# Kernel optimization log

Measured on AMD Instinct MI355X. Metric: run time of the kernel, lower is better.

The kernel has to match this reference:

```python
import jax, jax.numpy as jnp
import numpy as np

B, N, C, H, NC = 8, 4096, 512, 256, 1000
GRID = 64  # N = GRID*GRID unique positions
LN_EPS = 1e-5


def setup_inputs() -> dict:
    key = jax.random.key(0)
    ks = jax.random.split(key, 10)
    # unique integer grid positions, same for every batch element (original order)
    i = jnp.arange(N)
    base = jnp.stack([i % GRID, i // GRID], axis=-1).astype(jnp.float32)  # [N,2]
    pos_org = jnp.broadcast_to(base, (B, N, 2))
    # per-batch random permutation -> shuffled positions (as the backbone would emit)
    perm = jax.vmap(lambda k: jax.random.permutation(k, N))(jax.random.split(ks[0], B))  # [B,N]
    pos_shuffled = jnp.take_along_axis(pos_org, perm[..., None], axis=1)
    s = 0.02
    return {
        "feat": jax.random.normal(ks[1], (B, N, C), jnp.float32),
        "prev_out": jax.random.normal(ks[2], (B, N, C), jnp.float32),
        "pos_org": pos_org,
        "pos_shuffled": pos_shuffled,
        "proj_W": jax.random.normal(ks[3], (C, C), jnp.float32) * s,
        "proj_b": jnp.zeros((C,), jnp.float32),
        "ln_g": jnp.ones((C,), jnp.float32),
        "ln_b": jnp.zeros((C,), jnp.float32),
        "W1": jax.random.normal(ks[4], (H, C), jnp.float32) * s,
        "b1": jnp.zeros((H,), jnp.float32),
        "W2": jax.random.normal(ks[5], (H, H), jnp.float32) * s,
        "b2": jnp.zeros((H,), jnp.float32),
        "W3": jax.random.normal(ks[6], (NC, H), jnp.float32) * s,
        "b3": jnp.zeros((NC,), jnp.float32),
    }


def _layernorm(x, g, b):
    x32 = x.astype(jnp.float32)
    mu = x32.mean(-1, keepdims=True)
    var = ((x32 - mu) ** 2).mean(-1, keepdims=True)
    return (x32 - mu) * jax.lax.rsqrt(var + LN_EPS) * g + b


def reference(feat, prev_out, pos_org, pos_shuffled, proj_W, proj_b,
              ln_g, ln_b, W1, b1, W2, b2, W3, b3):
    # find_pos_org_order: L1 cdist [B,N,N] + argmin over shuffled axis
    dists = jnp.abs(pos_org[:, :, None, :] - pos_shuffled[:, None, :, :]).sum(-1)
    pos_indices = jnp.argmin(dists, axis=2)  # [B,N]
    # batched gather: feat[b_, pos_indices]
    g = jnp.take_along_axis(feat, pos_indices[..., None], axis=1)  # [B,N,C]
    # fused proj -> layernorm (in fp32) -> cast back -> residual add
    proj = jnp.einsum('bnc,dc->bnd', g, proj_W) + proj_b
    out_feat = prev_out + _layernorm(proj, ln_g, ln_b).astype(feat.dtype)
    # mean-pool over tokens, 3-layer MLP head with relu on first two layers
    pooled = out_feat.mean(1)  # [B,C]
    h = jax.nn.relu(pooled @ W1.T + b1)
    h = jax.nn.relu(h @ W2.T + b2)
    return h @ W3.T + b3  # [B, num_classes]
```

## Files before the change

kernel.cpp:

```cpp
#include <hip/hip_runtime.h>
#include <stdint.h>

#define B_ 8
#define N_ 4096
#define C_ 512
#define H_ 256
#define NC_ 1000

typedef float v4f __attribute__((ext_vector_type(4)));
typedef short v8s __attribute__((ext_vector_type(8)));
typedef unsigned short ushort_t;

__device__ __forceinline__ uint32_t f2bf1(float f) {
    uint32_t u = __float_as_uint(f);
    return (u + 0x7FFFu + ((u >> 16) & 1u)) >> 16;
}
__device__ __forceinline__ uint32_t pk2(float lo, float hi) {
#if __has_builtin(__builtin_amdgcn_cvt_pk_bf16_f32)
    auto r = __builtin_amdgcn_cvt_pk_bf16_f32(lo, hi);
    return __builtin_bit_cast(uint32_t, r);
#else
    return f2bf1(lo) | (f2bf1(hi) << 16);
#endif
}

__global__ void prep_kernel(const float* __restrict__ ps, const float* __restrict__ W,
                            int* __restrict__ inv, ushort_t* __restrict__ Wfrag,
                            float* __restrict__ pooled) {
    int blk = blockIdx.x, t = threadIdx.x;
    if (blk == 0) {
        float4 z = {0.f, 0.f, 0.f, 0.f};
#pragma unroll
        for (int i = 0; i < 4; i++) ((float4*)pooled)[t * 4 + i] = z;
    }
    if (blk < 128) {
        int gid = blk * 256 + t;
        float2 p = ((const float2*)ps)[gid];
        int key = (int)(p.x + 0.5f) + 64 * (int)(p.y + 0.5f);
        int b = gid >> 12;
        inv[(b << 12) + key] = gid & 4095;
    } else {
        int i = (blk - 128) * 256 + t;
        int d = i >> 6, kb = (i >> 2) & 15, q = i & 3;
        const float4* src = (const float4*)(W + d * C_ + kb * 32 + q * 8);
        float4 v0 = src[0], v1 = src[1];
        uint4 pk;
        pk.x = pk2(v0.x, v0.y); pk.y = pk2(v0.z, v0.w);
        pk.z = pk2(v1.x, v1.y); pk.w = pk2(v1.z, v1.w);
        ((uint4*)Wfrag)[((d >> 4) * 16 + kb) * 64 + q * 16 + (d & 15)] = pk;
    }
}

__global__ __launch_bounds__(512, 4)
void gemm_ln_pool(const float* __restrict__ feat, const float* __restrict__ prev,
                  const int* __restrict__ inv, const ushort_t* __restrict__ Wfrag,
                  const float* __restrict__ pb, const float* __restrict__ lg,
                  const float* __restrict__ lb, float* __restrict__ pooled) {
    __shared__ v8s Abuf[4096];
    __shared__ float RowS[64], RowQ[64], ColS[512];

    const int bid = blockIdx.x;
    const int t = threadIdx.x;

    if (bid % 3 == 2) {
        const int p = bid / 3;
        const int b = p >> 5;
        const int r0 = (p & 31) << 7;
        const float* psrc = prev + ((size_t)(b * N_ + r0) * C_) + t;
        float s0 = 0.f, s1 = 0.f, s2 = 0.f, s3 = 0.f;
#pragma unroll 4
        for (int r = 0; r < 128; r += 4) {
            s0 += psrc[(r + 0) * C_];
            s1 += psrc[(r + 1) * C_];
            s2 += psrc[(r + 2) * C_];
            s3 += psrc[(r + 3) * C_];
        }
        atomicAdd(&pooled[b * C_ + t], (s0 + s1) + (s2 + s3));
        return;
    }

    const int gix = (bid / 3) * 2 + (bid % 3);
    const int b = gix >> 6;
    const int row0 = (gix & 63) << 6;
    const int wv = t >> 6, lane = t & 63, c = lane & 15, q = lane >> 4;

    if (t < 64) { RowS[t] = 0.f; RowQ[t] = 0.f; }

    const int arow = t >> 3;
    const int acol8 = t & 7;
    const int grow = inv[(b << 12) + row0 + arow];
    const float* asrc = feat + ((size_t)(b * N_ + grow) * C_);
#pragma unroll 4
    for (int s = 0; s < 8; s++) {
        const int chunk = s * 8 + acol8;
        float4 f0 = ((const float4*)asrc)[chunk * 2];
        float4 f1 = ((const float4*)asrc)[chunk * 2 + 1];
        uint4 pk;
        pk.x = pk2(f0.x, f0.y); pk.y = pk2(f0.z, f0.w);
        pk.z = pk2(f1.x, f1.y); pk.w = pk2(f1.z, f1.w);
        ((uint4*)Abuf)[arow * 64 + (chunk ^ (arow & 7))] = pk;
    }

    const ushort_t* fb[4];
#pragma unroll
    for (int nt = 0; nt < 4; nt++)
        fb[nt] = Wfrag + (wv * 4 + nt) * 8192 + lane * 8;

    v4f acc[4][4];
    const v4f vzero = {0.f, 0.f, 0.f, 0.f};
#pragma unroll
    for (int mt = 0; mt < 4; mt++)
#pragma unroll
        for (int nt = 0; nt < 4; nt++) acc[mt][nt] = vzero;

    __syncthreads();

#pragma unroll 2
    for (int kb = 0; kb < 16; kb++) {
        v8s af[4], bf[4];
#pragma unroll
        for (int nt = 0; nt < 4; nt++)
            bf[nt] = *((const v8s*)(fb[nt] + kb * 512));
#pragma unroll
        for (int mt = 0; mt < 4; mt++)
            af[mt] = Abuf[(mt * 16 + c) * 64 + ((kb * 4 + q) ^ (c & 7))];
#pragma unroll
        for (int mt = 0; mt < 4; mt++)
#pragma unroll
            for (int nt = 0; nt < 4; nt++)
                acc[mt][nt] = __builtin_amdgcn_mfma_f32_16x16x32_bf16(
                    af[mt], bf[nt], acc[mt][nt], 0, 0, 0);
    }

    float pb4[4], lg4[4], lb4[4];
#pragma unroll
    for (int nt = 0; nt < 4; nt++) {
        int n = wv * 64 + nt * 16 + c;
        pb4[nt] = pb[n]; lg4[nt] = lg[n]; lb4[nt] = lb[n];
    }
#pragma unroll
    for (int mt = 0; mt < 4; mt++) {
#pragma unroll
        for (int reg = 0; reg < 4; reg++) {
            float s1 = 0.f, s2 = 0.f;
#pragma unroll
            for (int nt = 0; nt < 4; nt++) {
                float v = acc[mt][nt][reg] + pb4[nt];
                acc[mt][nt][reg] = v;
                s1 += v; s2 += v * v;
            }
#pragma unroll
            for (int d = 1; d < 16; d <<= 1) {
                s1 += __shfl_xor(s1, d);
                s2 += __shfl_xor(s2, d);
            }
            if (c == 0) {
                int r = mt * 16 + q * 4 + reg;
                atomicAdd(&RowS[r], s1);
                atomicAdd(&RowQ[r], s2);
            }
        }
    }
    __syncthreads();
    if (t < 64) {
        float mu = RowS[t] * (1.f / C_);
        float var = RowQ[t] * (1.f / C_) - mu * mu;
        RowS[t] = mu;
        RowQ[t] = rsqrtf(var + 1e-5f);
    }
    __syncthreads();
    float col[4] = {0.f, 0.f, 0.f, 0.f};
#pragma unroll
    for (int mt = 0; mt < 4; mt++) {
#pragma unroll
        for (int reg = 0; reg < 4; reg++) {
            int r = mt * 16 + q * 4 + reg;
            float mu = RowS[r], rs = RowQ[r];
#pragma unroll
            for (int nt = 0; nt < 4; nt++)
                col[nt] += (acc[mt][nt][reg] - mu) * rs * lg4[nt] + lb4[nt];
        }
    }
#pragma unroll
    for (int nt = 0; nt < 4; nt++) {
        col[nt] += __shfl_xor(col[nt], 16);
        col[nt] += __shfl_xor(col[nt], 32);
    }
    if (lane < 16) {
#pragma unroll
        for (int nt = 0; nt < 4; nt++) ColS[wv * 64 + nt * 16 + c] = col[nt];
    }
    __syncthreads();
    atomicAdd(&pooled[b * C_ + t], ColS[t]);
}

__global__ __launch_bounds__(256)
void head_kernel(const float* __restrict__ pooled,
                 const float* __restrict__ W1, const float* __restrict__ b1,
                 const float* __restrict__ W2, const float* __restrict__ b2,
                 const float* __restrict__ W3, const float* __restrict__ b3,
                 float* __restrict__ out) {
    __shared__ __align__(16) float P[512];
    __shared__ __align__(16) float H1[256];
    __shared__ __align__(16) float H2[256];
    const int t = threadIdx.x, wv = t >> 6, lane = t & 63;
    const int b = blockIdx.x / 25;
    const int slice = blockIdx.x % 25;

    P[t] = pooled[b * C_ + t] * (1.f / 4096.f);
    P[t + 256] = pooled[b * C_ + t + 256] * (1.f / 4096.f);
    __syncthreads();

    {
        const float4* wr = (const float4*)(W1 + t * C_);
        float s = 0.f;
#pragma unroll 8
        for (int k = 0; k < 128; k++) {
            float4 w = wr[k];
            float4 p = ((const float4*)P)[k];
            s += w.x * p.x + w.y * p.y + w.z * p.z + w.w * p.w;
        }
        H1[t] = fmaxf(s + b1[t], 0.f);
    }
    __syncthreads();

    {
        const float4* wr = (const float4*)(W2 + t * H_);
        float s = 0.f;
#pragma unroll 8
        for (int k = 0; k < 64; k++) {
            float4 w = wr[k];
            float4 p = ((const float4*)H1)[k];
            s += w.x * p.x + w.y * p.y + w.z * p.z + w.w * p.w;
        }
        H2[t] = fmaxf(s + b2[t], 0.f);
    }
    __syncthreads();

#pragma unroll
    for (int jj = 0; jj < 10; jj++) {
        const int o = slice * 40 + jj * 4 + wv;
        float4 w = ((const float4*)(W3 + o * H_))[lane];
        float4 p = ((const float4*)H2)[lane];
        float s = w.x * p.x + w.y * p.y + w.z * p.z + w.w * p.w;
#pragma unroll
        for (int d = 1; d < 64; d <<= 1) s += __shfl_xor(s, d);
        if (lane == 0) out[b * NC_ + o] = s + b3[o];
    }
}

extern "C" void kernel_launch(void* const* d_in, const int* in_sizes, int n_in,
                              void* d_out, int out_size, void* d_ws, size_t ws_size,
                              hipStream_t stream) {
    const float* feat  = (const float*)d_in[0];
    const float* prev  = (const float*)d_in[1];
    const float* ps    = (const float*)d_in[3];
    const float* projW = (const float*)d_in[4];
    const float* pb    = (const float*)d_in[5];
    const float* lg    = (const float*)d_in[6];
    const float* lb    = (const float*)d_in[7];
    const float* W1    = (const float*)d_in[8];
    const float* b1    = (const float*)d_in[9];
    const float* W2    = (const float*)d_in[10];
    const float* b2    = (const float*)d_in[11];
    const float* W3    = (const float*)d_in[12];
    const float* b3    = (const float*)d_in[13];
    float* out = (float*)d_out;

    char* ws = (char*)d_ws;
    ushort_t* Wfrag = (ushort_t*)ws;
    int* inv        = (int*)(ws + 524288);
    float* pooled   = (float*)(ws + 655360);

    prep_kernel<<<256, 256, 0, stream>>>(ps, projW, inv, Wfrag, pooled);
    gemm_ln_pool<<<768, 512, 0, stream>>>(feat, prev, inv, Wfrag,
                                          pb, lg, lb, pooled);
    head_kernel<<<200, 256, 0, stream>>>(pooled, W1, b1, W2, b2, W3, b3, out);
}
```

Baseline: 220.1 us.

## Fuse prev_out pooling into GEMM blocks and double-buffer weight fragment loads

Drops the dedicated prev_out summing blocks. Each GEMM block now sums its own 64 prev_out rows with vectorized loads issued alongside the A-tile staging, reduces them through shared-memory atomics, and folds the result into its single global atomic per column. The K loop is fully unrolled and prefetches the next weight fragments into a second register buffer, overlapping global loads with MFMA work. The grid shrinks from 768 to 512 blocks. This adds register pressure and per-block memory traffic, which could hurt occupancy.

```diff
diff --git a/kernel.cpp b/kernel.cpp
--- a/kernel.cpp
+++ b/kernel.cpp
@@ -57,34 +57,16 @@
                   const float* __restrict__ pb, const float* __restrict__ lg,
                   const float* __restrict__ lb, float* __restrict__ pooled) {
     __shared__ v8s Abuf[4096];
-    __shared__ float RowS[64], RowQ[64], ColS[512];
+    __shared__ float RowS[64], RowQ[64], ColS[512], ColPrev[512];
 
     const int bid = blockIdx.x;
     const int t = threadIdx.x;
-
-    if (bid % 3 == 2) {
-        const int p = bid / 3;
-        const int b = p >> 5;
-        const int r0 = (p & 31) << 7;
-        const float* psrc = prev + ((size_t)(b * N_ + r0) * C_) + t;
-        float s0 = 0.f, s1 = 0.f, s2 = 0.f, s3 = 0.f;
-#pragma unroll 4
-        for (int r = 0; r < 128; r += 4) {
-            s0 += psrc[(r + 0) * C_];
-            s1 += psrc[(r + 1) * C_];
-            s2 += psrc[(r + 2) * C_];
-            s3 += psrc[(r + 3) * C_];
-        }
-        atomicAdd(&pooled[b * C_ + t], (s0 + s1) + (s2 + s3));
-        return;
-    }
-
-    const int gix = (bid / 3) * 2 + (bid % 3);
-    const int b = gix >> 6;
-    const int row0 = (gix & 63) << 6;
+    const int b = bid >> 6;
+    const int row0 = (bid & 63) << 6;
     const int wv = t >> 6, lane = t & 63, c = lane & 15, q = lane >> 4;
 
     if (t < 64) { RowS[t] = 0.f; RowQ[t] = 0.f; }
+    ColPrev[t] = 0.f;
 
     const int arow = t >> 3;
     const int acol8 = t & 7;
@@ -101,6 +83,12 @@
         ((uint4*)Abuf)[arow * 64 + (chunk ^ (arow & 7))] = pk;
     }
 
+    const int pcol = t & 127, rg = t >> 7;
+    const v4f* psrc = (const v4f*)(prev + (size_t)(b * N_ + row0 + rg * 16) * C_) + pcol;
+    v4f psum = {0.f, 0.f, 0.f, 0.f};
+#pragma unroll 8
+    for (int r = 0; r < 16; r++) psum += psrc[r * 128];
+
     const ushort_t* fb[4];
 #pragma unroll
     for (int nt = 0; nt < 4; nt++)
@@ -113,14 +101,25 @@
 #pragma unroll
         for (int nt = 0; nt < 4; nt++) acc[mt][nt] = vzero;
 
-    __syncthreads();
-
-#pragma unroll 2
+    v8s bf[2][4], af[4];
+#pragma unroll
+    for (int nt = 0; nt < 4; nt++) bf[0][nt] = *((const v8s*)(fb[nt]));
+
+    __syncthreads();
+
+    atomicAdd(&ColPrev[pcol * 4 + 0], psum.x);
+    atomicAdd(&ColPrev[pcol * 4 + 1], psum.y);
+    atomicAdd(&ColPrev[pcol * 4 + 2], psum.z);
+    atomicAdd(&ColPrev[pcol * 4 + 3], psum.w);
+
+#pragma unroll
     for (int kb = 0; kb < 16; kb++) {
-        v8s af[4], bf[4];
-#pragma unroll
-        for (int nt = 0; nt < 4; nt++)
-            bf[nt] = *((const v8s*)(fb[nt] + kb * 512));
+        const int cur = kb & 1;
+        if (kb < 15) {
+#pragma unroll
+            for (int nt = 0; nt < 4; nt++)
+                bf[cur ^ 1][nt] = *((const v8s*)(fb[nt] + (kb + 1) * 512));
+        }
 #pragma unroll
         for (int mt = 0; mt < 4; mt++)
             af[mt] = Abuf[(mt * 16 + c) * 64 + ((kb * 4 + q) ^ (c & 7))];
@@ -129,7 +128,7 @@
 #pragma unroll
             for (int nt = 0; nt < 4; nt++)
                 acc[mt][nt] = __builtin_amdgcn_mfma_f32_16x16x32_bf16(
-                    af[mt], bf[nt], acc[mt][nt], 0, 0, 0);
+                    af[mt], bf[cur][nt], acc[mt][nt], 0, 0, 0);
     }
 
     float pb4[4], lg4[4], lb4[4];
@@ -191,7 +190,7 @@
         for (int nt = 0; nt < 4; nt++) ColS[wv * 64 + nt * 16 + c] = col[nt];
     }
     __syncthreads();
-    atomicAdd(&pooled[b * C_ + t], ColS[t]);
+    atomicAdd(&pooled[b * C_ + t], ColS[t] + ColPrev[t]);
 }
 
 __global__ __launch_bounds__(256)
@@ -273,7 +272,7 @@
     float* pooled   = (float*)(ws + 655360);
 
     prep_kernel<<<256, 256, 0, stream>>>(ps, projW, inv, Wfrag, pooled);
-    gemm_ln_pool<<<768, 512, 0, stream>>>(feat, prev, inv, Wfrag,
+    gemm_ln_pool<<<512, 512, 0, stream>>>(feat, prev, inv, Wfrag,
                                           pb, lg, lb, pooled);
     head_kernel<<<200, 256, 0, stream>>>(pooled, W1, b1, W2, b2, W3, b3, out);
 }
```

Measured after the change: 230.2 us. +4.6%, slower.
